# Optimization experiments

Measured on AMD Instinct MI355X. Metric: run time of the kernel, lower is better.

The kernel has to match this reference:

```python
import jax, jax.numpy as jnp
import numpy as np

BATCH = 1024
INPUT_DIM = 4096
HIDDEN_DIM = 4096
N_BLOCKS = 8
BLOCK_SIZE = HIDDEN_DIM // N_BLOCKS          # 512
IN_BLOCK_SIZE = INPUT_DIM // N_BLOCKS        # 512


def setup_inputs() -> dict:
    key = jax.random.key(0)
    ks = jax.random.split(key, 6)
    scale = 1.0 / np.sqrt(BLOCK_SIZE)  # torch GRUCell init: U(-1/sqrt(hidden), 1/sqrt(hidden))
    return {
        "x": jax.random.normal(ks[0], (BATCH, INPUT_DIM), dtype=jnp.float32),
        "h": jax.random.normal(ks[1], (BATCH, HIDDEN_DIM), dtype=jnp.float32),
        "W_ih": jax.random.normal(ks[2], (N_BLOCKS, 3 * BLOCK_SIZE, IN_BLOCK_SIZE), dtype=jnp.float32) * scale,
        "W_hh": jax.random.normal(ks[3], (N_BLOCKS, 3 * BLOCK_SIZE, BLOCK_SIZE), dtype=jnp.float32) * scale,
        "b_ih": jax.random.normal(ks[4], (N_BLOCKS, 3 * BLOCK_SIZE), dtype=jnp.float32) * scale,
        "b_hh": jax.random.normal(ks[5], (N_BLOCKS, 3 * BLOCK_SIZE), dtype=jnp.float32) * scale,
    }


def reference(x, h, W_ih, W_hh, b_ih, b_hh):
    B = x.shape[0]
    n, g3, ibs = W_ih.shape           # n_blocks, 3*block_size, input_block_size
    bs = W_hh.shape[2]                # block_size
    xb = x.reshape(B, n, ibs)         # (B, n_blocks, input_block_size)
    hb = h.reshape(B, n, bs)          # (B, n_blocks, block_size)
    # Block-diagonal GEMM: one grouped matmul over all blocks at once.
    gi = jnp.einsum('bni,ngi->bng', xb, W_ih) + b_ih   # (B, n, 3*bs)
    gh = jnp.einsum('bnh,ngh->bng', hb, W_hh) + b_hh   # (B, n, 3*bs)
    i_r, i_z, i_n = jnp.split(gi, 3, axis=-1)
    h_r, h_z, h_n = jnp.split(gh, 3, axis=-1)
    r = jax.nn.sigmoid(i_r + h_r)                      # reset gate
    z = jax.nn.sigmoid(i_z + h_z)                      # update gate
    n_gate = jnp.tanh(i_n + r * h_n)                   # candidate state
    new_h = n_gate + z * (hb - n_gate)                 # torch GRUCell: h' = (1-z)*n + z*h
    return new_h.reshape(B, n * bs)
```

## Files before the change

### kernel.cpp

```cpp
#include <hip/hip_runtime.h>
#include <hip/hip_bf16.h>
#include <stdint.h>

#define G1CAST(p) ((const __attribute__((address_space(1))) void*)(p))
#define L3CAST(p) ((__attribute__((address_space(3))) void*)(p))

typedef short bf16x8 __attribute__((ext_vector_type(8)));
typedef float f32x16 __attribute__((ext_vector_type(16)));

static __device__ __forceinline__ short f2bf(float f) {
    __hip_bfloat16 b = __float2bfloat16(f);
    return __builtin_bit_cast(short, b);
}

__global__ __launch_bounds__(256) void wconv_kernel(const float* __restrict__ Wih,
                                                    const float* __restrict__ Whh,
                                                    short* __restrict__ Wcat) {
    const int tid = blockIdx.x * 256 + threadIdx.x;
    const int64_t e = (int64_t)tid * 8;
    const int kk = (int)(e & 1023);
    const int row = (int)(e >> 10);
    const int n = row / 1536;
    const int gr = row - n * 1536;
    const float* src = (kk < 512)
        ? Wih + ((int64_t)n * 786432 + (int64_t)gr * 512 + kk)
        : Whh + ((int64_t)n * 786432 + (int64_t)gr * 512 + (kk - 512));
    const float4 a = ((const float4*)src)[0];
    const float4 b = ((const float4*)src)[1];
    bf16x8 o;
    o[0] = f2bf(a.x); o[1] = f2bf(a.y); o[2] = f2bf(a.z); o[3] = f2bf(a.w);
    o[4] = f2bf(b.x); o[5] = f2bf(b.y); o[6] = f2bf(b.z); o[7] = f2bf(b.w);
    *(bf16x8*)(Wcat + e) = o;
}

__global__ __launch_bounds__(256) void aconv_kernel(const float* __restrict__ x,
                                                    const float* __restrict__ h,
                                                    short* __restrict__ Aimg) {
    const int gid = blockIdx.x * 256 + threadIdx.x;
    const int c4 = gid & 3;
    const int r = (gid >> 2) & 255;
    const int tile = gid >> 10;
    const int ks = tile & 31;
    const int nblk = (tile >> 5) & 7;
    const int bt = tile >> 8;
    const float* base = (ks < 16) ? x : h;
    const float* src = base + ((size_t)(bt * 256 + r) * 4096
                               + nblk * 512 + (ks & 15) * 32 + c4 * 8);
    const float4 a = ((const float4*)src)[0];
    const float4 b = ((const float4*)src)[1];
    bf16x8 o;
    o[0] = f2bf(a.x); o[1] = f2bf(a.y); o[2] = f2bf(a.z); o[3] = f2bf(a.w);
    o[4] = f2bf(b.x); o[5] = f2bf(b.y); o[6] = f2bf(b.z); o[7] = f2bf(b.w);
    *(bf16x8*)(Aimg + (size_t)tile * 8192 + r * 32 + ((c4 ^ ((r >> 1) & 3)) * 8)) = o;
}

__global__ __launch_bounds__(512, 2) void gru_kernel(
    const float* __restrict__ hst,
    const short* __restrict__ Wcat, const short* __restrict__ Aimg,
    const float* __restrict__ b_ih, const float* __restrict__ b_hh,
    float* __restrict__ out)
{
    __shared__ short ldsA[4][8192];
    __shared__ short ldsB[4][8192];

    const int tid = threadIdx.x;
    const int nblk = blockIdx.x & 7;
    const int rr_ = blockIdx.x >> 3;
    const int bt = rr_ >> 3;
    const int jt = rr_ & 7;
    const int j0b = jt * 64;
    const int brow0 = bt * 256;

    const int lane = tid & 63;
    const int wave = tid >> 6;
    const int wm = wave >> 1;
    const int wn = wave & 1;
    const int l31 = lane & 31;
    const int k8 = lane >> 5;

    auto bsrc_of = [&](int c) -> size_t {
        const int g = c >> 8, j = (c & 255) >> 2, ci = c & 3;
        return ((size_t)nblk * 1536 + (size_t)g * 512 + (size_t)(j0b + j)) * 1024
             + (size_t)((ci ^ ((j >> 1) & 3)) * 8);
    };
    const size_t bsrc0 = bsrc_of(tid);
    const size_t bsrc1 = bsrc_of(tid < 256 ? tid + 512 : tid + 256);
    const size_t a_tile0 = ((size_t)(bt * 8 + nblk) * 32) << 14;

    f32x16 acc_r[2] = {};
    f32x16 acc_z[2] = {};
    f32x16 acc_nx[2] = {};
    f32x16 acc_nh[2] = {};

    auto stage = [&](int buf, int ks) {
        const char* asrc = (const char*)Aimg + a_tile0 + ((size_t)ks << 14) + (size_t)tid * 16;
        char* adst = (char*)&ldsA[buf][0] + tid * 16;
        __builtin_amdgcn_global_load_lds(G1CAST(asrc), L3CAST(adst), 16, 0, 0);
        __builtin_amdgcn_global_load_lds(G1CAST(asrc + 8192), L3CAST(adst + 8192), 16, 0, 0);
        const short* ws = Wcat + (size_t)ks * 32;
        char* bdst = (char*)&ldsB[buf][0] + tid * 16;
        __builtin_amdgcn_global_load_lds(G1CAST(ws + bsrc0), L3CAST(bdst), 16, 0, 0);
        __builtin_amdgcn_global_load_lds(G1CAST(ws + bsrc1), L3CAST(bdst + 8192), 16, 0, 0);
    };

    const int jl = wn * 32 + l31;
    const int boff = jl * 64;
    const int bswz = ((jl >> 1) & 3) << 4;
    const int arow0 = wm * 64 + l31;
    const int arow1 = arow0 + 32;
    const int aoff0 = arow0 * 64;
    const int aoff1 = arow1 * 64;
    const int aswz0 = ((arow0 >> 1) & 3) << 4;
    const int aswz1 = ((arow1 >> 1) & 3) << 4;

    auto computeStep = [&](const short* Ab_s, const short* Bb_s, f32x16 (&accN)[2]) {
        const char* Ab = (const char*)Ab_s;
        const char* Bb = (const char*)Bb_s;
        #pragma unroll
        for (int ksub = 0; ksub < 2; ++ksub) {
            const int kb = ksub * 32 + k8 * 16;
            bf16x8 af0 = *(const bf16x8*)(Ab + aoff0 + (kb ^ aswz0));
            bf16x8 af1 = *(const bf16x8*)(Ab + aoff1 + (kb ^ aswz1));
            bf16x8 b0 = *(const bf16x8*)(Bb + 0 * 4096 + boff + (kb ^ bswz));
            bf16x8 b1 = *(const bf16x8*)(Bb + 1 * 4096 + boff + (kb ^ bswz));
            bf16x8 b2 = *(const bf16x8*)(Bb + 2 * 4096 + boff + (kb ^ bswz));
            acc_r[0] = __builtin_amdgcn_mfma_f32_32x32x16_bf16(af0, b0, acc_r[0], 0, 0, 0);
            acc_r[1] = __builtin_amdgcn_mfma_f32_32x32x16_bf16(af1, b0, acc_r[1], 0, 0, 0);
            acc_z[0] = __builtin_amdgcn_mfma_f32_32x32x16_bf16(af0, b1, acc_z[0], 0, 0, 0);
            acc_z[1] = __builtin_amdgcn_mfma_f32_32x32x16_bf16(af1, b1, acc_z[1], 0, 0, 0);
            accN[0]  = __builtin_amdgcn_mfma_f32_32x32x16_bf16(af0, b2, accN[0], 0, 0, 0);
            accN[1]  = __builtin_amdgcn_mfma_f32_32x32x16_bf16(af1, b2, accN[1], 0, 0, 0);
        }
    };

    stage(0, 0); stage(1, 1); stage(2, 2);

    #pragma unroll 1
    for (int i = 0; i < 16; ++i) {
        asm volatile("s_waitcnt vmcnt(8)" ::: "memory");
        __builtin_amdgcn_sched_barrier(0);
        __builtin_amdgcn_s_barrier();
        stage((i + 3) & 3, i + 3);
        computeStep(ldsA[i & 3], ldsB[i & 3], acc_nx);
    }
    #pragma unroll 1
    for (int i = 16; i < 29; ++i) {
        asm volatile("s_waitcnt vmcnt(8)" ::: "memory");
        __builtin_amdgcn_sched_barrier(0);
        __builtin_amdgcn_s_barrier();
        stage((i + 3) & 3, i + 3);
        computeStep(ldsA[i & 3], ldsB[i & 3], acc_nh);
    }
    asm volatile("s_waitcnt vmcnt(8)" ::: "memory");
    __builtin_amdgcn_sched_barrier(0);
    __builtin_amdgcn_s_barrier();
    computeStep(ldsA[29 & 3], ldsB[29 & 3], acc_nh);
    asm volatile("s_waitcnt vmcnt(4)" ::: "memory");
    __builtin_amdgcn_sched_barrier(0);
    __builtin_amdgcn_s_barrier();
    computeStep(ldsA[30 & 3], ldsB[30 & 3], acc_nh);
    asm volatile("s_waitcnt vmcnt(0)" ::: "memory");
    __builtin_amdgcn_sched_barrier(0);
    __builtin_amdgcn_s_barrier();
    computeStep(ldsA[31 & 3], ldsB[31 & 3], acc_nh);

    const int jb = j0b + wn * 32 + l31;
    const int bb = nblk * 1536 + jb;
    const float br = b_ih[bb] + b_hh[bb];
    const float bz = b_ih[bb + 512] + b_hh[bb + 512];
    const float bnx = b_ih[bb + 1024];
    const float bnh = b_hh[bb + 1024];
    const int gcol = nblk * 512 + jb;
    #pragma unroll
    for (int m = 0; m < 2; ++m) {
        #pragma unroll
        for (int rr = 0; rr < 16; ++rr) {
            const int rowl = (rr & 3) + 8 * (rr >> 2) + 4 * k8;
            const int row = brow0 + wm * 64 + m * 32 + rowl;
            const size_t idx = (size_t)row * 4096 + gcol;
            const float sr = acc_r[m][rr] + br;
            const float sz = acc_z[m][rr] + bz;
            const float rg = 1.f / (1.f + __expf(-sr));
            const float zg = 1.f / (1.f + __expf(-sz));
            const float tin = (acc_nx[m][rr] + bnx) + rg * (acc_nh[m][rr] + bnh);
            const float e2 = __expf(-2.f * tin);
            const float ng = 2.f / (1.f + e2) - 1.f;
            const float hv = hst[idx];
            out[idx] = ng + zg * (hv - ng);
        }
    }
}

extern "C" void kernel_launch(void* const* d_in, const int* in_sizes, int n_in,
                              void* d_out, int out_size, void* d_ws, size_t ws_size,
                              hipStream_t stream) {
    (void)in_sizes; (void)n_in; (void)out_size; (void)ws_size;
    const float* x    = (const float*)d_in[0];
    const float* h    = (const float*)d_in[1];
    const float* W_ih = (const float*)d_in[2];
    const float* W_hh = (const float*)d_in[3];
    const float* b_ih = (const float*)d_in[4];
    const float* b_hh = (const float*)d_in[5];
    short* Wcat = (short*)d_ws;
    short* Aimg = (short*)d_ws + (size_t)12 * 1024 * 1024;

    wconv_kernel<<<6144, 256, 0, stream>>>(W_ih, W_hh, Wcat);
    aconv_kernel<<<4096, 256, 0, stream>>>(x, h, Aimg);
    gru_kernel<<<256, 512, 0, stream>>>(h, Wcat, Aimg, b_ih, b_hh, (float*)d_out);
}
```

Before: 69.95 us.

## Halve batch tile to 128 rows, deepen K step to 64, double-buffer LDS

```diff
diff --git a/kernel.cpp b/kernel.cpp
--- a/kernel.cpp
+++ b/kernel.cpp
@@ -7,6 +7,10 @@
 
 typedef short bf16x8 __attribute__((ext_vector_type(8)));
 typedef float f32x16 __attribute__((ext_vector_type(16)));
+
+__device__ __host__ __forceinline__ int swz3(int r) {
+    return (r & 7) ^ (((r >> 3) & 1) << 2);
+}
 
 static __device__ __forceinline__ short f2bf(float f) {
     __hip_bfloat16 b = __float2bfloat16(f);
@@ -37,31 +41,31 @@
                                                     const float* __restrict__ h,
                                                     short* __restrict__ Aimg) {
     const int gid = blockIdx.x * 256 + threadIdx.x;
-    const int c4 = gid & 3;
-    const int r = (gid >> 2) & 255;
+    const int c4 = gid & 7;
+    const int r = (gid >> 3) & 127;
     const int tile = gid >> 10;
-    const int ks = tile & 31;
-    const int nblk = (tile >> 5) & 7;
-    const int bt = tile >> 8;
-    const float* base = (ks < 16) ? x : h;
-    const float* src = base + ((size_t)(bt * 256 + r) * 4096
-                               + nblk * 512 + (ks & 15) * 32 + c4 * 8);
+    const int ks = tile & 15;
+    const int nblk = (tile >> 4) & 7;
+    const int bt = tile >> 7;
+    const float* base = (ks < 8) ? x : h;
+    const float* src = base + ((size_t)(bt * 128 + r) * 4096
+                               + nblk * 512 + (ks & 7) * 64 + c4 * 8);
     const float4 a = ((const float4*)src)[0];
     const float4 b = ((const float4*)src)[1];
     bf16x8 o;
     o[0] = f2bf(a.x); o[1] = f2bf(a.y); o[2] = f2bf(a.z); o[3] = f2bf(a.w);
     o[4] = f2bf(b.x); o[5] = f2bf(b.y); o[6] = f2bf(b.z); o[7] = f2bf(b.w);
-    *(bf16x8*)(Aimg + (size_t)tile * 8192 + r * 32 + ((c4 ^ ((r >> 1) & 3)) * 8)) = o;
-}
-
-__global__ __launch_bounds__(512, 2) void gru_kernel(
+    *(bf16x8*)(Aimg + (size_t)tile * 8192 + r * 64 + (c4 ^ swz3(r)) * 8) = o;
+}
+
+__global__ __launch_bounds__(256, 2) void gru_kernel(
     const float* __restrict__ hst,
     const short* __restrict__ Wcat, const short* __restrict__ Aimg,
     const float* __restrict__ b_ih, const float* __restrict__ b_hh,
     float* __restrict__ out)
 {
-    __shared__ short ldsA[4][8192];
-    __shared__ short ldsB[4][8192];
+    __shared__ short ldsA[2][128 * 64];
+    __shared__ short ldsB[2][3 * 64 * 64];
 
     const int tid = threadIdx.x;
     const int nblk = blockIdx.x & 7;
@@ -69,7 +73,7 @@
     const int bt = rr_ >> 3;
     const int jt = rr_ & 7;
     const int j0b = jt * 64;
-    const int brow0 = bt * 256;
+    const int brow0 = bt * 128;
 
     const int lane = tid & 63;
     const int wave = tid >> 6;
@@ -78,14 +82,18 @@
     const int l31 = lane & 31;
     const int k8 = lane >> 5;
 
-    auto bsrc_of = [&](int c) -> size_t {
-        const int g = c >> 8, j = (c & 255) >> 2, ci = c & 3;
-        return ((size_t)nblk * 1536 + (size_t)g * 512 + (size_t)(j0b + j)) * 1024
-             + (size_t)((ci ^ ((j >> 1) & 3)) * 8);
-    };
-    const size_t bsrc0 = bsrc_of(tid);
-    const size_t bsrc1 = bsrc_of(tid < 256 ? tid + 512 : tid + 256);
-    const size_t a_tile0 = ((size_t)(bt * 8 + nblk) * 32) << 14;
+    uint32_t bsrc[6];
+    #pragma unroll
+    for (int u = 0; u < 6; ++u) {
+        const int q = tid + 256 * u;
+        const int g = q >> 9;
+        const int rem = q & 511;
+        const int j = rem >> 3;
+        const int c = rem & 7;
+        bsrc[u] = (uint32_t)(((nblk * 1536 + g * 512 + j0b + j) * 1024
+                              + (c ^ swz3(j)) * 8) * 2);
+    }
+    const size_t a_tile0 = ((size_t)(bt * 8 + nblk) << 18);
 
     f32x16 acc_r[2] = {};
     f32x16 acc_z[2] = {};
@@ -93,37 +101,36 @@
     f32x16 acc_nh[2] = {};
 
     auto stage = [&](int buf, int ks) {
-        const char* asrc = (const char*)Aimg + a_tile0 + ((size_t)ks << 14) + (size_t)tid * 16;
-        char* adst = (char*)&ldsA[buf][0] + tid * 16;
-        __builtin_amdgcn_global_load_lds(G1CAST(asrc), L3CAST(adst), 16, 0, 0);
-        __builtin_amdgcn_global_load_lds(G1CAST(asrc + 8192), L3CAST(adst + 8192), 16, 0, 0);
-        const short* ws = Wcat + (size_t)ks * 32;
-        char* bdst = (char*)&ldsB[buf][0] + tid * 16;
-        __builtin_amdgcn_global_load_lds(G1CAST(ws + bsrc0), L3CAST(bdst), 16, 0, 0);
-        __builtin_amdgcn_global_load_lds(G1CAST(ws + bsrc1), L3CAST(bdst + 8192), 16, 0, 0);
+        const char* as = (const char*)Aimg + a_tile0 + ((size_t)ks << 14) + (size_t)tid * 16;
+        char* ad = (char*)&ldsA[buf][0] + tid * 16;
+        #pragma unroll
+        for (int u = 0; u < 4; ++u)
+            __builtin_amdgcn_global_load_lds(G1CAST(as + u * 4096), L3CAST(ad + u * 4096), 16, 0, 0);
+        const char* wsb = (const char*)Wcat + (size_t)ks * 128;
+        char* bd = (char*)&ldsB[buf][0] + tid * 16;
+        #pragma unroll
+        for (int u = 0; u < 6; ++u)
+            __builtin_amdgcn_global_load_lds(G1CAST(wsb + bsrc[u]), L3CAST(bd + u * 4096), 16, 0, 0);
     };
 
-    const int jl = wn * 32 + l31;
-    const int boff = jl * 64;
-    const int bswz = ((jl >> 1) & 3) << 4;
     const int arow0 = wm * 64 + l31;
     const int arow1 = arow0 + 32;
-    const int aoff0 = arow0 * 64;
-    const int aoff1 = arow1 * 64;
-    const int aswz0 = ((arow0 >> 1) & 3) << 4;
-    const int aswz1 = ((arow1 >> 1) & 3) << 4;
+    const int jrow = wn * 32 + l31;
+    const int swA0 = swz3(arow0), swA1 = swz3(arow1), swB = swz3(jrow);
+    const int abase0 = arow0 * 128, abase1 = arow1 * 128;
+    const int bbase = jrow * 128;
 
     auto computeStep = [&](const short* Ab_s, const short* Bb_s, f32x16 (&accN)[2]) {
         const char* Ab = (const char*)Ab_s;
         const char* Bb = (const char*)Bb_s;
         #pragma unroll
-        for (int ksub = 0; ksub < 2; ++ksub) {
-            const int kb = ksub * 32 + k8 * 16;
-            bf16x8 af0 = *(const bf16x8*)(Ab + aoff0 + (kb ^ aswz0));
-            bf16x8 af1 = *(const bf16x8*)(Ab + aoff1 + (kb ^ aswz1));
-            bf16x8 b0 = *(const bf16x8*)(Bb + 0 * 4096 + boff + (kb ^ bswz));
-            bf16x8 b1 = *(const bf16x8*)(Bb + 1 * 4096 + boff + (kb ^ bswz));
-            bf16x8 b2 = *(const bf16x8*)(Bb + 2 * 4096 + boff + (kb ^ bswz));
+        for (int ksub = 0; ksub < 4; ++ksub) {
+            const int ch = ksub * 2 + k8;
+            bf16x8 af0 = *(const bf16x8*)(Ab + abase0 + ((ch ^ swA0) << 4));
+            bf16x8 af1 = *(const bf16x8*)(Ab + abase1 + ((ch ^ swA1) << 4));
+            bf16x8 b0 = *(const bf16x8*)(Bb + 0 * 8192 + bbase + ((ch ^ swB) << 4));
+            bf16x8 b1 = *(const bf16x8*)(Bb + 1 * 8192 + bbase + ((ch ^ swB) << 4));
+            bf16x8 b2 = *(const bf16x8*)(Bb + 2 * 8192 + bbase + ((ch ^ swB) << 4));
             acc_r[0] = __builtin_amdgcn_mfma_f32_32x32x16_bf16(af0, b0, acc_r[0], 0, 0, 0);
             acc_r[1] = __builtin_amdgcn_mfma_f32_32x32x16_bf16(af1, b0, acc_r[1], 0, 0, 0);
             acc_z[0] = __builtin_amdgcn_mfma_f32_32x32x16_bf16(af0, b1, acc_z[0], 0, 0, 0);
@@ -133,36 +140,24 @@
         }
     };
 
-    stage(0, 0); stage(1, 1); stage(2, 2);
+    stage(0, 0);
 
     #pragma unroll 1
-    for (int i = 0; i < 16; ++i) {
-        asm volatile("s_waitcnt vmcnt(8)" ::: "memory");
+    for (int i = 0; i < 8; ++i) {
+        asm volatile("s_waitcnt vmcnt(0)" ::: "memory");
         __builtin_amdgcn_sched_barrier(0);
         __builtin_amdgcn_s_barrier();
-        stage((i + 3) & 3, i + 3);
-        computeStep(ldsA[i & 3], ldsB[i & 3], acc_nx);
+        stage((i + 1) & 1, i + 1);
+        computeStep(ldsA[i & 1], ldsB[i & 1], acc_nx);
     }
     #pragma unroll 1
-    for (int i = 16; i < 29; ++i) {
-        asm volatile("s_waitcnt vmcnt(8)" ::: "memory");
+    for (int i = 8; i < 16; ++i) {
+        asm volatile("s_waitcnt vmcnt(0)" ::: "memory");
         __builtin_amdgcn_sched_barrier(0);
         __builtin_amdgcn_s_barrier();
-        stage((i + 3) & 3, i + 3);
-        computeStep(ldsA[i & 3], ldsB[i & 3], acc_nh);
-    }
-    asm volatile("s_waitcnt vmcnt(8)" ::: "memory");
-    __builtin_amdgcn_sched_barrier(0);
-    __builtin_amdgcn_s_barrier();
-    computeStep(ldsA[29 & 3], ldsB[29 & 3], acc_nh);
-    asm volatile("s_waitcnt vmcnt(4)" ::: "memory");
-    __builtin_amdgcn_sched_barrier(0);
-    __builtin_amdgcn_s_barrier();
-    computeStep(ldsA[30 & 3], ldsB[30 & 3], acc_nh);
-    asm volatile("s_waitcnt vmcnt(0)" ::: "memory");
-    __builtin_amdgcn_sched_barrier(0);
-    __builtin_amdgcn_s_barrier();
-    computeStep(ldsA[31 & 3], ldsB[31 & 3], acc_nh);
+        if (i < 15) stage((i + 1) & 1, i + 1);
+        computeStep(ldsA[i & 1], ldsB[i & 1], acc_nh);
+    }
 
     const int jb = j0b + wn * 32 + l31;
     const int bb = nblk * 1536 + jb;
@@ -206,5 +201,5 @@
 
     wconv_kernel<<<6144, 256, 0, stream>>>(W_ih, W_hh, Wcat);
     aconv_kernel<<<4096, 256, 0, stream>>>(x, h, Aimg);
-    gru_kernel<<<256, 512, 0, stream>>>(h, Wcat, Aimg, b_ih, b_hh, (float*)d_out);
-}
+    gru_kernel<<<512, 256, 0, stream>>>(h, Wcat, Aimg, b_ih, b_hh, (float*)d_out);
+}
```

Result: faster. 60.19 us (-14.0%).
